# Optimization experiments

Measured on AMD Instinct MI355X. Metric: run time of the kernel, lower is better.

Reference implementation:

```python
import jax, jax.numpy as jnp
import numpy as np

N, E, G = 30000, 60000, 1200
EMB, HID, OUT = 768, 384, 768
NEG = 0.01  # leaky_relu negative slope (torch default / GATConv negative_slope)


def _seg_softmax(a, idx, num):
    m = jax.ops.segment_max(a, idx, num_segments=num)
    e = jnp.exp(a - m[idx])
    s = jax.ops.segment_sum(e, idx, num_segments=num)
    return e / (s[idx] + 1e-16)


def _gru(x, h, Wi, Wh, bi, bh):
    gi = x @ Wi + bi
    gh = h @ Wh + bh
    ir, iz, in_ = jnp.split(gi, 3, -1)
    hr, hz, hn = jnp.split(gh, 3, -1)
    r = jax.nn.sigmoid(ir + hr)
    z = jax.nn.sigmoid(iz + hz)
    n = jnp.tanh(in_ + r * hn)
    return (1.0 - z) * n + z * h


def setup_inputs() -> dict:
    key = jax.random.key(0)
    ks = iter(jax.random.split(key, 64))
    def W(*shape):
        return jax.random.normal(next(ks), shape, jnp.float32) / np.sqrt(shape[0])
    z = lambda *s: jnp.zeros(s, jnp.float32)
    inp = {}
    inp['x_idx'] = jax.random.randint(next(ks), (N, 9), 0, 178)
    inp['edge_index'] = jax.random.randint(next(ks), (2, E), 0, N)
    inp['edge_attr_idx'] = jax.random.randint(next(ks), (E, 3), 0, 18)
    inp['batch'] = jnp.sort(jax.random.randint(next(ks), (N,), 0, G))
    inp['x_emb'] = W(178, EMB)
    inp['e_emb'] = W(18, EMB)
    inp['lin1_W'] = W(EMB, HID); inp['lin1_b'] = z(HID)
    inp['att_l'] = W(HID); inp['att_r'] = W(HID)
    inp['gl1_W'] = W(HID + EMB, HID); inp['gl2_W'] = W(HID, HID); inp['gate_b'] = z(HID)
    inp['gru1_Wi'] = W(HID, 3 * HID); inp['gru1_Wh'] = W(HID, 3 * HID)
    inp['gru1_bi'] = z(3 * HID); inp['gru1_bh'] = z(3 * HID)
    inp['gat_W'] = W(HID, HID); inp['gat_as'] = W(HID); inp['gat_ad'] = W(HID); inp['gat_b'] = z(HID)
    inp['gru2_Wi'] = W(HID, 3 * HID); inp['gru2_Wh'] = W(HID, 3 * HID)
    inp['gru2_bi'] = z(3 * HID); inp['gru2_bh'] = z(3 * HID)
    inp['mol_W'] = W(HID, HID); inp['mol_as'] = W(HID); inp['mol_ad'] = W(HID); inp['mol_b'] = z(HID)
    inp['mgru_Wi'] = W(HID, 3 * HID); inp['mgru_Wh'] = W(HID, 3 * HID)
    inp['mgru_bi'] = z(3 * HID); inp['mgru_bh'] = z(3 * HID)
    inp['lin2_W'] = W(HID, OUT); inp['lin2_b'] = z(OUT)
    return inp


def reference(x_idx, edge_index, edge_attr_idx, batch,
              x_emb, e_emb, lin1_W, lin1_b,
              att_l, att_r, gl1_W, gl2_W, gate_b,
              gru1_Wi, gru1_Wh, gru1_bi, gru1_bh,
              gat_W, gat_as, gat_ad, gat_b,
              gru2_Wi, gru2_Wh, gru2_bi, gru2_bh,
              mol_W, mol_as, mol_ad, mol_b,
              mgru_Wi, mgru_Wh, mgru_bi, mgru_bh,
              lin2_W, lin2_b):
    src, dst = edge_index[0], edge_index[1]
    # embedding-sum over feature columns
    x = x_emb[x_idx].sum(1)            # [N, EMB]
    ea = e_emb[edge_attr_idx].sum(1)   # [E, EMB]
    x = jax.nn.leaky_relu(x @ lin1_W + lin1_b, NEG)  # [N, HID]
    # --- GATEConv (edge-attr attention) ---
    m = jax.nn.leaky_relu(jnp.concatenate([x[src], ea], -1) @ gl1_W, NEG)  # [E, HID]
    a = jax.nn.leaky_relu(m @ att_l + x[dst] @ att_r, NEG)
    a = _seg_softmax(a, dst, N)
    h = jax.ops.segment_sum((m @ gl2_W) * a[:, None], dst, num_segments=N) + gate_b
    x = jax.nn.relu(_gru(jax.nn.elu(h), x, gru1_Wi, gru1_Wh, gru1_bi, gru1_bh))
    # --- atom GATConv (num_layers=2 -> one extra layer, heads=1, no self-loops) ---
    xl = x @ gat_W
    a = jax.nn.leaky_relu((xl @ gat_as)[src] + (xl @ gat_ad)[dst], NEG)
    a = _seg_softmax(a, dst, N)
    h = jax.ops.segment_sum(xl[src] * a[:, None], dst, num_segments=N) + gat_b
    x = jax.nn.relu(_gru(jax.nn.elu(h), x, gru2_Wi, gru2_Wh, gru2_bi, gru2_bh))
    # --- attentive molecule readout, num_timesteps=3 ---
    out = jax.nn.relu(jax.ops.segment_sum(x, batch, num_segments=G))  # [G, HID]
    xl = x @ mol_W
    a_node = xl @ mol_as  # per-node source attention term (fixed across timesteps)
    for _ in range(3):
        a_g = (out @ mol_W) @ mol_ad
        a = jax.nn.leaky_relu(a_node + a_g[batch], NEG)
        a = _seg_softmax(a, batch, G)
        h = jax.ops.segment_sum(xl * a[:, None], batch, num_segments=G) + mol_b
        out = jax.nn.relu(_gru(jax.nn.elu(h), out, mgru_Wi, mgru_Wh, mgru_bi, mgru_bh))
    return out @ lin2_W + lin2_b  # [G, OUT]
```

## Files before the change

### kernel.cpp

```cpp
#include <hip/hip_runtime.h>
#include <cstdint>
#include <cstddef>

#define NN 30000
#define NE 60000
#define NG 1200
#define HID 384
#define EMB 768
#define OUTD 768
#define NEGS 0.01f

typedef _Float16 f16;
typedef _Float16 f16x8 __attribute__((ext_vector_type(8)));
typedef float f32x16 __attribute__((ext_vector_type(16)));

static __device__ __forceinline__ float leaky(float x){ return x > 0.f ? x : NEGS * x; }
static __device__ __forceinline__ float elu1(float x){ return x > 0.f ? x : (expf(x) - 1.f); }
static __device__ __forceinline__ float sigm(float x){ return 1.f / (1.f + expf(-x)); }

static __device__ __forceinline__ size_t pf_idx(int row, int col){
  return (((((size_t)(row >> 5)) * 24 + (col >> 4)) * 2 + ((col >> 3) & 1)) * 32
          + (row & 31)) * 8 + (col & 7);
}
#define PF_RB_STRIDE 12288
#define PF_KS_STRIDE 512
#define PF_GATE_STRIDE 147456

__global__ __launch_bounds__(256) void k_gemm(
    const float* __restrict__ A, const float* __restrict__ B,
    const float* __restrict__ bias, float* __restrict__ C,
    int M, int N, int K, int act)
{
  __shared__ float As[16][65];
  __shared__ float Bs[16][65];
  const int tid = threadIdx.x;
  const int tx = tid & 15, ty = tid >> 4;
  const int row0 = blockIdx.y * 64, col0 = blockIdx.x * 64;
  const int ar = tid >> 2, ak = (tid & 3) << 2;
  const int bk = tid >> 4, bc = (tid & 15) << 2;
  float acc[4][4] = {};
  for (int k0 = 0; k0 < K; k0 += 16) {
    float4 av = make_float4(0.f, 0.f, 0.f, 0.f);
    if (row0 + ar < M)
      av = *(const float4*)(A + (size_t)(row0 + ar) * K + k0 + ak);
    As[ak + 0][ar] = av.x; As[ak + 1][ar] = av.y;
    As[ak + 2][ar] = av.z; As[ak + 3][ar] = av.w;
    float4 bv = *(const float4*)(B + (size_t)(k0 + bk) * N + col0 + bc);
    Bs[bk][bc + 0] = bv.x; Bs[bk][bc + 1] = bv.y;
    Bs[bk][bc + 2] = bv.z; Bs[bk][bc + 3] = bv.w;
    __syncthreads();
#pragma unroll
    for (int kk = 0; kk < 16; kk++) {
      float a[4], b[4];
#pragma unroll
      for (int i = 0; i < 4; i++) a[i] = As[kk][(ty << 2) + i];
#pragma unroll
      for (int j = 0; j < 4; j++) b[j] = Bs[kk][(tx << 2) + j];
#pragma unroll
      for (int i = 0; i < 4; i++)
#pragma unroll
        for (int j = 0; j < 4; j++)
          acc[i][j] = fmaf(a[i], b[j], acc[i][j]);
    }
    __syncthreads();
  }
#pragma unroll
  for (int i = 0; i < 4; i++) {
    int r = row0 + (ty << 2) + i;
    if (r >= M) continue;
#pragma unroll
    for (int j = 0; j < 4; j++) {
      int c = col0 + (tx << 2) + j;
      float v = acc[i][j];
      if (bias) v += bias[c];
      if (act == 1) v = leaky(v);
      else if (act == 2) v = elu1(v);
      else if (act == 3) v = fmaxf(v, 0.f);
      C[(size_t)r * N + c] = v;
    }
  }
}

__global__ __launch_bounds__(256) void k_hgemm(
    const f16* __restrict__ Apf, const f16* __restrict__ Bpf,
    const float* __restrict__ bias, float* __restrict__ Cf, f16* __restrict__ Ch,
    int M, int Nn, int act)
{
  const int nct = Nn >> 7;
  const int id = blockIdx.x;
  const int lane8 = id & 7, chunk = id >> 3;
  const int ct = chunk % nct, rg = chunk / nct;
  const int rt = rg * 8 + lane8;
  const int Mt = (M + 127) >> 7;
  if (rt >= Mt) return;
  const int r0 = rt * 128, n0 = ct * 128;
  const int tid = threadIdx.x;
  const int wid = tid >> 6, lane = tid & 63;
  const int wr = wid >> 1, wc = wid & 1;
  const int l31 = lane & 31, lhi = lane >> 5;
  const size_t lane_off = (size_t)(lhi * 32 + l31) * 8;
  const f16* pA[2]; const f16* pB[2];
#pragma unroll
  for (int i = 0; i < 2; i++) {
    pA[i] = Apf + (size_t)(r0 / 32 + wr * 2 + i) * PF_RB_STRIDE + lane_off;
    pB[i] = Bpf + (size_t)(n0 / 32 + wc * 2 + i) * PF_RB_STRIDE + lane_off;
  }
  f32x16 acc[2][2];
#pragma unroll
  for (int i = 0; i < 2; i++)
#pragma unroll
    for (int j = 0; j < 2; j++)
#pragma unroll
      for (int r = 0; r < 16; r++) acc[i][j][r] = 0.f;
  f16x8 af[2], bf[2], naf[2], nbf[2];
#pragma unroll
  for (int i = 0; i < 2; i++) { af[i] = *(const f16x8*)(pA[i]); bf[i] = *(const f16x8*)(pB[i]); }
#pragma unroll 4
  for (int ks = 0; ks < 24; ks++) {
    const size_t noff = (size_t)(ks < 23 ? ks + 1 : 23) * PF_KS_STRIDE;
#pragma unroll
    for (int i = 0; i < 2; i++) { naf[i] = *(const f16x8*)(pA[i] + noff); nbf[i] = *(const f16x8*)(pB[i] + noff); }
#pragma unroll
    for (int i = 0; i < 2; i++)
#pragma unroll
      for (int j = 0; j < 2; j++)
        acc[i][j] = __builtin_amdgcn_mfma_f32_32x32x16_f16(af[i], bf[j], acc[i][j], 0, 0, 0);
#pragma unroll
    for (int i = 0; i < 2; i++) { af[i] = naf[i]; bf[i] = nbf[i]; }
  }
#pragma unroll
  for (int i = 0; i < 2; i++)
#pragma unroll
    for (int j = 0; j < 2; j++) {
      int col = n0 + wc * 64 + j * 32 + l31;
      float bv = bias ? bias[col] : 0.f;
#pragma unroll
      for (int r = 0; r < 16; r++) {
        int row = r0 + wr * 64 + i * 32 + (r & 3) + 8 * (r >> 2) + 4 * lhi;
        if (row < M) {
          float v = acc[i][j][r] + bv;
          if (act == 1) v = leaky(v);
          else if (act == 2) v = elu1(v);
          else if (act == 3) v = fmaxf(v, 0.f);
          if (Cf) Cf[(size_t)row * Nn + col] = v;
          if (Ch) Ch[pf_idx(row, col)] = (f16)v;
        }
      }
    }
}

__global__ __launch_bounds__(256) void k_gru_hgemm(
    const f16* __restrict__ Upf, const f16* __restrict__ Hpf,
    const f16* __restrict__ Wip, const f16* __restrict__ Whp,
    const float* __restrict__ bi, const float* __restrict__ bh,
    float* __restrict__ Xo, f16* __restrict__ Xoh, int M)
{
  const int id = blockIdx.x;
  const int lane8 = id & 7, chunk = id >> 3;
  const int ct = chunk % 6, rg = chunk / 6;
  const int rt = rg * 8 + lane8;
  const int Mt = (M + 63) >> 6;
  if (rt >= Mt) return;
  const int r0 = rt * 64, c0 = ct * 64;
  const int tid = threadIdx.x;
  const int wid = tid >> 6, lane = tid & 63;
  const int wr = wid >> 1, wc = wid & 1;
  const int l31 = lane & 31, lhi = lane >> 5;
  const size_t lane_off = (size_t)(lhi * 32 + l31) * 8;
  const f16* pU  = Upf + (size_t)(r0 / 32 + wr) * PF_RB_STRIDE + lane_off;
  const f16* pH  = Hpf + (size_t)(r0 / 32 + wr) * PF_RB_STRIDE + lane_off;
  const f16* pWi = Wip + (size_t)(c0 / 32 + wc) * PF_RB_STRIDE + lane_off;
  const f16* pWh = Whp + (size_t)(c0 / 32 + wc) * PF_RB_STRIDE + lane_off;
#define Z16 {0,0,0,0,0,0,0,0,0,0,0,0,0,0,0,0}
  f32x16 accR = Z16, accZ = Z16, aN = Z16, hN = Z16;
  f16x8 au, ah, bir, biz, bin, bhr, bhz, bhn;
  f16x8 nau, nah, nbir, nbiz, nbin, nbhr, nbhz, nbhn;
  au  = *(const f16x8*)(pU);
  ah  = *(const f16x8*)(pH);
  bir = *(const f16x8*)(pWi);
  biz = *(const f16x8*)(pWi + PF_GATE_STRIDE);
  bin = *(const f16x8*)(pWi + 2 * PF_GATE_STRIDE);
  bhr = *(const f16x8*)(pWh);
  bhz = *(const f16x8*)(pWh + PF_GATE_STRIDE);
  bhn = *(const f16x8*)(pWh + 2 * PF_GATE_STRIDE);
#pragma unroll 4
  for (int ks = 0; ks < 24; ks++) {
    const size_t noff = (size_t)(ks < 23 ? ks + 1 : 23) * PF_KS_STRIDE;
    nau  = *(const f16x8*)(pU + noff);
    nah  = *(const f16x8*)(pH + noff);
    nbir = *(const f16x8*)(pWi + noff);
    nbiz = *(const f16x8*)(pWi + PF_GATE_STRIDE + noff);
    nbin = *(const f16x8*)(pWi + 2 * PF_GATE_STRIDE + noff);
    nbhr = *(const f16x8*)(pWh + noff);
    nbhz = *(const f16x8*)(pWh + PF_GATE_STRIDE + noff);
    nbhn = *(const f16x8*)(pWh + 2 * PF_GATE_STRIDE + noff);
    accR = __builtin_amdgcn_mfma_f32_32x32x16_f16(au, bir, accR, 0, 0, 0);
    accR = __builtin_amdgcn_mfma_f32_32x32x16_f16(ah, bhr, accR, 0, 0, 0);
    accZ = __builtin_amdgcn_mfma_f32_32x32x16_f16(au, biz, accZ, 0, 0, 0);
    accZ = __builtin_amdgcn_mfma_f32_32x32x16_f16(ah, bhz, accZ, 0, 0, 0);
    aN   = __builtin_amdgcn_mfma_f32_32x32x16_f16(au, bin, aN, 0, 0, 0);
    hN   = __builtin_amdgcn_mfma_f32_32x32x16_f16(ah, bhn, hN, 0, 0, 0);
    au = nau; ah = nah; bir = nbir; biz = nbiz; bin = nbin;
    bhr = nbhr; bhz = nbhz; bhn = nbhn;
  }
  const int col = c0 + wc * 32 + l31;
  const float brz = bi[col] + bh[col];
  const float bzz = bi[HID + col] + bh[HID + col];
  const float bin_ = bi[2 * HID + col];
  const float bhn_ = bh[2 * HID + col];
#pragma unroll
  for (int r = 0; r < 16; r++) {
    int row = r0 + wr * 32 + (r & 3) + 8 * (r >> 2) + 4 * lhi;
    if (row < M) {
      float rg_ = sigm(accR[r] + brz);
      float zg  = sigm(accZ[r] + bzz);
      float ng  = tanhf(aN[r] + bin_ + rg_ * (hN[r] + bhn_));
      float hp  = (float)Hpf[pf_idx(row, col)];
      float o = (1.f - zg) * ng + zg * hp;
      o = fmaxf(o, 0.f);
      if (Xo) Xo[(size_t)row * HID + col] = o;
      Xoh[pf_idx(row, col)] = (f16)o;
    }
  }
}

__global__ void k_wpack_all(
    const float* __restrict__ w0, const float* __restrict__ w1,
    const float* __restrict__ w2, const float* __restrict__ w3,
    const float* __restrict__ w4, const float* __restrict__ w5,
    const float* __restrict__ w6, const float* __restrict__ w7,
    const float* __restrict__ w8, const float* __restrict__ w9,
    const float* __restrict__ w10,
    f16* __restrict__ d0, f16* __restrict__ d1, f16* __restrict__ d2,
    f16* __restrict__ d3, f16* __restrict__ d4, f16* __restrict__ d5,
    f16* __restrict__ d6, f16* __restrict__ d7, f16* __restrict__ d8,
    f16* __restrict__ d9, f16* __restrict__ d10)
{
  long t = (long)blockIdx.x * blockDim.x + threadIdx.x;
  if (t >= 3538944L) return;
  const float* W; f16* Wp; int Nn; long tt;
  if (t < 589824L) {
    int s = (int)(t / 147456L); tt = t - (long)s * 147456L; Nn = HID;
    if (s == 0) { W = w0; Wp = d0; } else if (s == 1) { W = w1; Wp = d1; }
    else if (s == 2) { W = w2; Wp = d2; } else { W = w3; Wp = d3; }
  } else if (t < 3244032L) {
    long u = t - 589824L;
    int s = (int)(u / 442368L); tt = u - (long)s * 442368L; Nn = 3 * HID;
    if (s == 0) { W = w4; Wp = d4; } else if (s == 1) { W = w5; Wp = d5; }
    else if (s == 2) { W = w6; Wp = d6; } else if (s == 3) { W = w7; Wp = d7; }
    else if (s == 4) { W = w8; Wp = d8; } else { W = w9; Wp = d9; }
  } else {
    tt = t - 3244032L; Nn = OUTD; W = w10; Wp = d10;
  }
  int elem = (int)(tt & 7); long c = tt >> 3;
  int l31 = (int)(c & 31); long q = c >> 5;
  int lhi = (int)(q & 1); long p = q >> 1;
  int ks = (int)(p % 24); int rb = (int)(p / 24);
  int n = rb * 32 + l31, k = ks * 16 + lhi * 8 + elem;
  Wp[tt] = (f16)W[(size_t)k * Nn + n];
}

__global__ void k_node_embed2(const int* __restrict__ xi, const float* __restrict__ T1,
                              const float* __restrict__ b, const float* __restrict__ att_r,
                              f16* __restrict__ x1h, float* __restrict__ xr, int n)
{
  int w = (int)(((long)blockIdx.x * blockDim.x + threadIdx.x) >> 6);
  int lane = threadIdx.x & 63;
  if (w >= n) return;
  int idx[9];
#pragma unroll
  for (int j = 0; j < 9; j++) idx[j] = xi[w * 9 + j];
  float s = 0.f;
#pragma unroll
  for (int t = 0; t < 6; t++) {
    int c = lane + 64 * t;
    float v = b[c];
#pragma unroll
    for (int j = 0; j < 9; j++) v += T1[(size_t)idx[j] * HID + c];
    v = leaky(v);
    x1h[pf_idx(w, c)] = (f16)v;
    s += v * att_r[c];
  }
  for (int o = 32; o; o >>= 1) s += __shfl_down(s, o, 64);
  if (lane == 0) xr[w] = s;
}

__global__ void k_rowdot(const float* __restrict__ X, const float* __restrict__ v,
                         float* __restrict__ out, int M)
{
  int w = (int)(((long)blockIdx.x * blockDim.x + threadIdx.x) >> 6);
  int lane = threadIdx.x & 63;
  if (w >= M) return;
  float s = 0.f;
  for (int j = lane; j < HID; j += 64) s += X[(size_t)w * HID + j] * v[j];
  for (int o = 32; o; o >>= 1) s += __shfl_down(s, o, 64);
  if (lane == 0) out[w] = s;
}

__global__ void k_rowdot2(const float* __restrict__ X, const float* __restrict__ v1,
                          const float* __restrict__ v2, float* __restrict__ o1,
                          float* __restrict__ o2, int M)
{
  int w = (int)(((long)blockIdx.x * blockDim.x + threadIdx.x) >> 6);
  int lane = threadIdx.x & 63;
  if (w >= M) return;
  float s1 = 0.f, s2 = 0.f;
  for (int j = lane; j < HID; j += 64) {
    float x = X[(size_t)w * HID + j];
    s1 += x * v1[j]; s2 += x * v2[j];
  }
  for (int o = 32; o; o >>= 1) { s1 += __shfl_down(s1, o, 64); s2 += __shfl_down(s2, o, 64); }
  if (lane == 0) { o1[w] = s1; o2[w] = s2; }
}

__global__ void k_gbounds(const int* __restrict__ batch, int* __restrict__ gstart, int n, int G)
{
  int g = (int)((long)blockIdx.x * blockDim.x + threadIdx.x);
  if (g > G) return;
  int lo = 0, hi = n;
  while (lo < hi) { int mid = (lo + hi) >> 1; if (batch[mid] < g) lo = mid + 1; else hi = mid; }
  gstart[g] = lo;
}

__global__ void k_deg(const int* __restrict__ dst, int* __restrict__ cnt, int ne)
{
  int e = (int)((long)blockIdx.x * blockDim.x + threadIdx.x);
  if (e >= ne) return;
  atomicAdd(&cnt[dst[e]], 1);
}

__global__ __launch_bounds__(1024) void k_scan(const int* __restrict__ cnt,
                                               int* __restrict__ rowptr,
                                               int* __restrict__ cursor)
{
  __shared__ int part[1024];
  const int tid = threadIdx.x;
  const int c0 = tid * 30, c1 = min(c0 + 30, NN);
  int s = 0;
  for (int i = c0; i < c1; i++) s += cnt[i];
  part[tid] = s;
  __syncthreads();
  for (int o = 1; o < 1024; o <<= 1) {
    int v = (tid >= o) ? part[tid - o] : 0;
    __syncthreads();
    part[tid] += v;
    __syncthreads();
  }
  int run = (tid ? part[tid - 1] : 0);
  for (int i = c0; i < c1; i++) { rowptr[i] = run; cursor[i] = run; run += cnt[i]; }
  if (tid == 1023) rowptr[NN] = part[1023];
}

__global__ void k_fill(const int* __restrict__ dst, int* __restrict__ cursor,
                       int* __restrict__ elist, int ne)
{
  int e = (int)((long)blockIdx.x * blockDim.x + threadIdx.x);
  if (e >= ne) return;
  int p = atomicAdd(&cursor[dst[e]], 1);
  elist[p] = e;
}

__global__ void k_gate_agg(const float* __restrict__ P, const float* __restrict__ Te,
                           const int* __restrict__ ei, const int* __restrict__ eai,
                           const float* __restrict__ attl, const float* __restrict__ xr,
                           const int* __restrict__ rowptr, const int* __restrict__ elist,
                           f16* __restrict__ Hout, int n)
{
  int node = (int)(((long)blockIdx.x * blockDim.x + threadIdx.x) >> 6);
  int lane = threadIdx.x & 63;
  if (node >= n) return;
  const int e0 = rowptr[node], e1 = rowptr[node + 1];
  const float xrd = xr[node];
  float h0 = 0.f, h1 = 0.f, h2 = 0.f, h3 = 0.f, h4 = 0.f, h5 = 0.f;
  float mx = -3.4e38f, s = 0.f;
  for (int q = e0; q < e1; q++) {
    int e = elist[q];
    int src = ei[e];
    int i0 = eai[e * 3], i1 = eai[e * 3 + 1], i2 = eai[e * 3 + 2];
    float m[6];
    float dot = 0.f;
#pragma unroll
    for (int t = 0; t < 6; t++) {
      int c = lane + 64 * t;
      float v = P[(size_t)src * HID + c] + Te[(size_t)i0 * HID + c]
              + Te[(size_t)i1 * HID + c] + Te[(size_t)i2 * HID + c];
      v = leaky(v);
      m[t] = v;
      dot += v * attl[c];
    }
#pragma unroll
    for (int o = 32; o; o >>= 1) dot += __shfl_xor(dot, o, 64);
    float a = leaky(dot + xrd);
    if (a > mx) {
      float f = expf(mx - a);
      s *= f; h0 *= f; h1 *= f; h2 *= f; h3 *= f; h4 *= f; h5 *= f;
      mx = a;
    }
    float w = expf(a - mx);
    s += w;
    h0 += w * m[0]; h1 += w * m[1]; h2 += w * m[2];
    h3 += w * m[3]; h4 += w * m[4]; h5 += w * m[5];
  }
  const float inv = 1.f / (s + 1e-16f);
  Hout[pf_idx(node, lane)]           = (f16)(h0 * inv);
  Hout[pf_idx(node, lane + 64)]      = (f16)(h1 * inv);
  Hout[pf_idx(node, lane + 128)]     = (f16)(h2 * inv);
  Hout[pf_idx(node, lane + 192)]     = (f16)(h3 * inv);
  Hout[pf_idx(node, lane + 256)]     = (f16)(h4 * inv);
  Hout[pf_idx(node, lane + 320)]     = (f16)(h5 * inv);
}

__global__ void k_gat_agg(const float* __restrict__ XL, const int* __restrict__ ei,
                          const float* __restrict__ sS, const float* __restrict__ sD,
                          const float* __restrict__ gat_b,
                          const int* __restrict__ rowptr, const int* __restrict__ elist,
                          f16* __restrict__ Hout, int n)
{
  int node = (int)(((long)blockIdx.x * blockDim.x + threadIdx.x) >> 6);
  int lane = threadIdx.x & 63;
  if (node >= n) return;
  const int e0 = rowptr[node], e1 = rowptr[node + 1];
  const float sDn = sD[node];
  float h0 = 0.f, h1 = 0.f, h2 = 0.f, h3 = 0.f, h4 = 0.f, h5 = 0.f;
  float mx = -3.4e38f, s = 0.f;
  for (int q = e0; q < e1; q++) {
    int e = elist[q];
    int src = ei[e];
    float a = leaky(sS[src] + sDn);
    if (a > mx) {
      float f = expf(mx - a);
      s *= f; h0 *= f; h1 *= f; h2 *= f; h3 *= f; h4 *= f; h5 *= f;
      mx = a;
    }
    float w = expf(a - mx);
    s += w;
    const float* row = XL + (size_t)src * HID;
    h0 += w * row[lane];
    h1 += w * row[lane + 64];
    h2 += w * row[lane + 128];
    h3 += w * row[lane + 192];
    h4 += w * row[lane + 256];
    h5 += w * row[lane + 320];
  }
  const float inv = 1.f / (s + 1e-16f);
  Hout[pf_idx(node, lane)]       = (f16)elu1(h0 * inv + gat_b[lane]);
  Hout[pf_idx(node, lane + 64)]  = (f16)elu1(h1 * inv + gat_b[lane + 64]);
  Hout[pf_idx(node, lane + 128)] = (f16)elu1(h2 * inv + gat_b[lane + 128]);
  Hout[pf_idx(node, lane + 192)] = (f16)elu1(h3 * inv + gat_b[lane + 192]);
  Hout[pf_idx(node, lane + 256)] = (f16)elu1(h4 * inv + gat_b[lane + 256]);
  Hout[pf_idx(node, lane + 320)] = (f16)elu1(h5 * inv + gat_b[lane + 320]);
}

__global__ __launch_bounds__(384) void k_graph_sum(const float* __restrict__ X,
                                                   const int* __restrict__ gstart,
                                                   float* __restrict__ OUTa,
                                                   f16* __restrict__ OUTaPF)
{
  const int g = blockIdx.x;
  const int tid = threadIdx.x;
  const int s0 = gstart[g], s1 = gstart[g + 1];
  float acc = 0.f;
  for (int i = s0; i < s1; i++) acc += X[(size_t)i * HID + tid];
  acc = fmaxf(acc, 0.f);
  OUTa[(size_t)g * HID + tid] = acc;
  OUTaPF[pf_idx(g, tid)] = (f16)acc;
}

__global__ __launch_bounds__(384) void k_mol_iter(
    const float* __restrict__ cur, const float* __restrict__ XLm,
    const float* __restrict__ a_node, const float* __restrict__ w_g,
    const float* __restrict__ mol_b, const int* __restrict__ gstart,
    f16* __restrict__ HMp)
{
  const int g = blockIdx.x;
  const int tid = threadIdx.x;
  const int lane = tid & 63, wv = tid >> 6;
  __shared__ float red[6];
  __shared__ float wbuf[384];
  __shared__ float sh[3];
  const int s0 = gstart[g], s1 = gstart[g + 1];
  float p = cur[(size_t)g * HID + tid] * w_g[tid];
  for (int o = 32; o; o >>= 1) p += __shfl_down(p, o, 64);
  if (lane == 0) red[wv] = p;
  __syncthreads();
  if (tid == 0) { float s = 0.f; for (int i = 0; i < 6; i++) s += red[i]; sh[0] = s; }
  __syncthreads();
  const float ag = sh[0];
  float mx = -3.4e38f;
  for (int n = s0 + tid; n < s1; n += 384) mx = fmaxf(mx, leaky(a_node[n] + ag));
  for (int o = 32; o; o >>= 1) mx = fmaxf(mx, __shfl_down(mx, o, 64));
  __syncthreads();
  if (lane == 0) red[wv] = mx;
  __syncthreads();
  if (tid == 0) { float m = red[0]; for (int i = 1; i < 6; i++) m = fmaxf(m, red[i]); sh[1] = m; }
  __syncthreads();
  const float gmx = sh[1];
  float sm = 0.f;
  for (int n = s0 + tid; n < s1; n += 384) sm += expf(leaky(a_node[n] + ag) - gmx);
  for (int o = 32; o; o >>= 1) sm += __shfl_down(sm, o, 64);
  __syncthreads();
  if (lane == 0) red[wv] = sm;
  __syncthreads();
  if (tid == 0) { float s = 0.f; for (int i = 0; i < 6; i++) s += red[i]; sh[2] = s; }
  __syncthreads();
  const float inv = 1.f / (sh[2] + 1e-16f);
  float h = 0.f;
  for (int base = s0; base < s1; base += 384) {
    int cnt = min(384, s1 - base);
    __syncthreads();
    if (tid < cnt) wbuf[tid] = expf(leaky(a_node[base + tid] + ag) - gmx) * inv;
    __syncthreads();
    for (int k = 0; k < cnt; k++) h += XLm[(size_t)(base + k) * HID + tid] * wbuf[k];
  }
  h = elu1(h + mol_b[tid]);
  HMp[pf_idx(g, tid)] = (f16)h;
}

extern "C" void kernel_launch(void* const* d_in, const int* in_sizes, int n_in,
                              void* d_out, int out_size, void* d_ws, size_t ws_size,
                              hipStream_t stream)
{
  const int* x_idx = (const int*)d_in[0];
  const int* edge_index = (const int*)d_in[1];
  const int* eai = (const int*)d_in[2];
  const int* batch = (const int*)d_in[3];
  const float* x_emb = (const float*)d_in[4];
  const float* e_emb = (const float*)d_in[5];
  const float* lin1_W = (const float*)d_in[6];
  const float* lin1_b = (const float*)d_in[7];
  const float* att_l = (const float*)d_in[8];
  const float* att_r = (const float*)d_in[9];
  const float* gl1_W = (const float*)d_in[10];
  const float* gl2_W = (const float*)d_in[11];
  const float* gate_b = (const float*)d_in[12];
  const float* gru1_Wi = (const float*)d_in[13];
  const float* gru1_Wh = (const float*)d_in[14];
  const float* gru1_bi = (const float*)d_in[15];
  const float* gru1_bh = (const float*)d_in[16];
  const float* gat_W = (const float*)d_in[17];
  const float* gat_as = (const float*)d_in[18];
  const float* gat_ad = (const float*)d_in[19];
  const float* gat_b = (const float*)d_in[20];
  const float* gru2_Wi = (const float*)d_in[21];
  const float* gru2_Wh = (const float*)d_in[22];
  const float* gru2_bi = (const float*)d_in[23];
  const float* gru2_bh = (const float*)d_in[24];
  const float* mol_W = (const float*)d_in[25];
  const float* mol_as = (const float*)d_in[26];
  const float* mol_ad = (const float*)d_in[27];
  const float* mol_b = (const float*)d_in[28];
  const float* mgru_Wi = (const float*)d_in[29];
  const float* mgru_Wh = (const float*)d_in[30];
  const float* mgru_bi = (const float*)d_in[31];
  const float* mgru_bh = (const float*)d_in[32];
  const float* lin2_W = (const float*)d_in[33];
  const float* lin2_b = (const float*)d_in[34];
  float* outp = (float*)d_out;

  const size_t NB = (size_t)NN * HID;
  const size_t GB = (size_t)NG * HID;
  const size_t PFH = (size_t)940 * PF_RB_STRIDE;
  const size_t PFG = (size_t)40 * PF_RB_STRIDE;

  float* ws = (float*)d_ws;
  size_t off = 0;
  auto alloc = [&](size_t n) { float* p = ws + off; off += n; return p; };
  auto alloch = [&](size_t n) { f16* p = (f16*)(ws + off); off += (n + 1) / 2; return p; };
  float* A    = alloc(NB);
  float* B    = alloc(NB);
  f16* H1 = alloch(PFH);
  f16* H2 = alloch(PFH);
  f16* H3 = alloch(PFH);
  f16* W1p   = alloch((size_t)HID * HID);
  f16* W2p   = alloch((size_t)HID * HID);
  f16* Wgatp = alloch((size_t)HID * HID);
  f16* Wmolp = alloch((size_t)HID * HID);
  f16* Wg1ip = alloch((size_t)3 * HID * HID);
  f16* Wg1hp = alloch((size_t)3 * HID * HID);
  f16* Wg2ip = alloch((size_t)3 * HID * HID);
  f16* Wg2hp = alloch((size_t)3 * HID * HID);
  f16* Wmgip = alloch((size_t)3 * HID * HID);
  f16* Wmghp = alloch((size_t)3 * HID * HID);
  f16* Wl2p  = alloch((size_t)HID * OUTD);
  f16* OUTaPF = alloch(PFG);
  f16* OUTbPF = alloch(PFG);
  f16* HMp    = alloch(PFG);
  float* T1   = alloc((size_t)178 * HID);
  float* Te   = alloc((size_t)18 * HID);
  float* w_g  = alloc(HID);
  float* xr   = alloc(NN);
  float* sS   = alloc(NN);
  float* sD   = alloc(NN);
  float* a_node = alloc(NN);
  float* OUTa = alloc(GB);
  float* OUTb = alloc(GB);
  int* gstart = (int*)alloc(NG + 2);
  int* cnt    = (int*)alloc(NN);
  int* rowptr = (int*)alloc(NN + 2);
  int* cursor = (int*)alloc(NN);
  int* elist  = (int*)alloc(NE);
  (void)n_in; (void)in_sizes; (void)out_size;
  if (ws_size < off * sizeof(float)) return;

  const int* dstArr = edge_index + NE;
  dim3 blk(256);
  auto g1 = [](long n) { return dim3((unsigned)((n + 255) / 256)); };
  auto gw = [](long waves) { return dim3((unsigned)((waves * 64 + 255) / 256)); };
  const int MtH = (NN + 127) / 128;
  const dim3 gH((unsigned)(8 * 3 * ((MtH + 7) / 8)));
  const int MtR = (NN + 63) / 64;
  const dim3 gR((unsigned)(8 * 6 * ((MtR + 7) / 8)));
  const int MtGH = (NG + 127) / 128;
  const dim3 gF((unsigned)(8 * 6 * ((MtGH + 7) / 8)));
  const int MtGR = (NG + 63) / 64;
  const dim3 gRG((unsigned)(8 * 6 * ((MtGR + 7) / 8)));

  hipLaunchKernelGGL(k_wpack_all, g1(3538944L), blk, 0, stream,
                     gl1_W, gl2_W, gat_W, mol_W,
                     gru1_Wi, gru1_Wh, gru2_Wi, gru2_Wh, mgru_Wi, mgru_Wh, lin2_W,
                     W1p, W2p, Wgatp, Wmolp,
                     Wg1ip, Wg1hp, Wg2ip, Wg2hp, Wmgip, Wmghp, Wl2p);
  hipLaunchKernelGGL(k_gemm, dim3(HID / 64, 3), blk, 0, stream,
                     x_emb, lin1_W, nullptr, T1, 178, HID, EMB, 0);
  hipLaunchKernelGGL(k_gemm, dim3(HID / 64, 1), blk, 0, stream,
                     e_emb, gl1_W + (size_t)HID * HID, nullptr, Te, 18, HID, EMB, 0);
  hipLaunchKernelGGL(k_rowdot, gw(HID), blk, 0, stream, mol_W, mol_ad, w_g, HID);
  hipLaunchKernelGGL(k_gbounds, g1(NG + 1), blk, 0, stream, batch, gstart, NN, NG);
  hipMemsetAsync(cnt, 0, NN * sizeof(int), stream);
  hipLaunchKernelGGL(k_deg, g1(NE), blk, 0, stream, dstArr, cnt, NE);
  hipLaunchKernelGGL(k_scan, dim3(1), dim3(1024), 0, stream, cnt, rowptr, cursor);
  hipLaunchKernelGGL(k_fill, g1(NE), blk, 0, stream, dstArr, cursor, elist, NE);

  hipLaunchKernelGGL(k_node_embed2, gw(NN), blk, 0, stream, x_idx, T1, lin1_b, att_r, H1, xr, NN);

  hipLaunchKernelGGL(k_hgemm, gH, blk, 0, stream, H1, W1p, nullptr, B, (f16*)nullptr, NN, HID, 0);
  hipLaunchKernelGGL(k_gate_agg, gw(NN), blk, 0, stream, B, Te, edge_index, eai, att_l, xr,
                     rowptr, elist, H2, NN);
  hipLaunchKernelGGL(k_hgemm, gH, blk, 0, stream, H2, W2p, gate_b, (float*)nullptr, H3, NN, HID, 2);
  hipLaunchKernelGGL(k_gru_hgemm, gR, blk, 0, stream, H3, H1, Wg1ip, Wg1hp,
                     gru1_bi, gru1_bh, (float*)nullptr, H2, NN);

  hipLaunchKernelGGL(k_hgemm, gH, blk, 0, stream, H2, Wgatp, nullptr, B, (f16*)nullptr, NN, HID, 0);
  hipLaunchKernelGGL(k_rowdot2, gw(NN), blk, 0, stream, B, gat_as, gat_ad, sS, sD, NN);
  hipLaunchKernelGGL(k_gat_agg, gw(NN), blk, 0, stream, B, edge_index, sS, sD, gat_b,
                     rowptr, elist, H1, NN);
  hipLaunchKernelGGL(k_gru_hgemm, gR, blk, 0, stream, H1, H2, Wg2ip, Wg2hp,
                     gru2_bi, gru2_bh, B, H3, NN);

  hipLaunchKernelGGL(k_graph_sum, dim3(NG), dim3(384), 0, stream, B, gstart, OUTa, OUTaPF);
  hipLaunchKernelGGL(k_hgemm, gH, blk, 0, stream, H3, Wmolp, nullptr, A, (f16*)nullptr, NN, HID, 0);
  hipLaunchKernelGGL(k_rowdot, gw(NN), blk, 0, stream, A, mol_as, a_node, NN);

  float* cur = OUTa;   f16* curPF = OUTaPF;
  float* nxt = OUTb;   f16* nxtPF = OUTbPF;
  for (int t = 0; t < 3; t++) {
    hipLaunchKernelGGL(k_mol_iter, dim3(NG), dim3(384), 0, stream,
                       cur, A, a_node, w_g, mol_b, gstart, HMp);
    hipLaunchKernelGGL(k_gru_hgemm, gRG, blk, 0, stream, HMp, curPF, Wmgip, Wmghp,
                       mgru_bi, mgru_bh, nxt, nxtPF, NG);
    float* tf = cur; cur = nxt; nxt = tf;
    f16* th = curPF; curPF = nxtPF; nxtPF = th;
  }

  hipLaunchKernelGGL(k_hgemm, gF, blk, 0, stream, curPF, Wl2p, lin2_b, outp, (f16*)nullptr, NG, OUTD, 0);
}
```

Baseline: 795.2 us.

## Fuse attention row-dot products into GEMM epilogue and deepen GRU A-prefetch

```diff
diff --git a/kernel.cpp b/kernel.cpp
--- a/kernel.cpp
+++ b/kernel.cpp
@@ -84,7 +84,9 @@
 __global__ __launch_bounds__(256) void k_hgemm(
     const f16* __restrict__ Apf, const f16* __restrict__ Bpf,
     const float* __restrict__ bias, float* __restrict__ Cf, f16* __restrict__ Ch,
-    int M, int Nn, int act)
+    int M, int Nn, int act,
+    const float* __restrict__ dv1, const float* __restrict__ dv2,
+    float* __restrict__ od1, float* __restrict__ od2)
 {
   const int nct = Nn >> 7;
   const int id = blockIdx.x;
@@ -147,6 +149,29 @@
         }
       }
     }
+  if (od1) {
+    const float w1a = dv1[n0 + wc * 64 + l31];
+    const float w1b = dv1[n0 + wc * 64 + 32 + l31];
+    const float w2a = dv2 ? dv2[n0 + wc * 64 + l31] : 0.f;
+    const float w2b = dv2 ? dv2[n0 + wc * 64 + 32 + l31] : 0.f;
+#pragma unroll
+    for (int i = 0; i < 2; i++)
+#pragma unroll
+      for (int r = 0; r < 16; r++) {
+        int row = r0 + wr * 64 + i * 32 + (r & 3) + 8 * (r >> 2) + 4 * lhi;
+        float p1 = acc[i][0][r] * w1a + acc[i][1][r] * w1b;
+        float p2 = acc[i][0][r] * w2a + acc[i][1][r] * w2b;
+#pragma unroll
+        for (int o = 16; o; o >>= 1) {
+          p1 += __shfl_xor(p1, o, 64);
+          p2 += __shfl_xor(p2, o, 64);
+        }
+        if (l31 == 0 && row < M) {
+          atomicAdd(&od1[row], p1);
+          if (od2) atomicAdd(&od2[row], p2);
+        }
+      }
+  }
 }
 
 __global__ __launch_bounds__(256) void k_gru_hgemm(
@@ -173,10 +198,11 @@
   const f16* pWh = Whp + (size_t)(c0 / 32 + wc) * PF_RB_STRIDE + lane_off;
 #define Z16 {0,0,0,0,0,0,0,0,0,0,0,0,0,0,0,0}
   f32x16 accR = Z16, accZ = Z16, aN = Z16, hN = Z16;
-  f16x8 au, ah, bir, biz, bin, bhr, bhz, bhn;
-  f16x8 nau, nah, nbir, nbiz, nbin, nbhr, nbhz, nbhn;
-  au  = *(const f16x8*)(pU);
-  ah  = *(const f16x8*)(pH);
+  f16x8 au0, ah0, au1, ah1, bir, biz, bin, bhr, bhz, bhn;
+  au0 = *(const f16x8*)(pU);
+  ah0 = *(const f16x8*)(pH);
+  au1 = *(const f16x8*)(pU + PF_KS_STRIDE);
+  ah1 = *(const f16x8*)(pH + PF_KS_STRIDE);
   bir = *(const f16x8*)(pWi);
   biz = *(const f16x8*)(pWi + PF_GATE_STRIDE);
   bin = *(const f16x8*)(pWi + 2 * PF_GATE_STRIDE);
@@ -185,22 +211,24 @@
   bhn = *(const f16x8*)(pWh + 2 * PF_GATE_STRIDE);
 #pragma unroll 4
   for (int ks = 0; ks < 24; ks++) {
-    const size_t noff = (size_t)(ks < 23 ? ks + 1 : 23) * PF_KS_STRIDE;
-    nau  = *(const f16x8*)(pU + noff);
-    nah  = *(const f16x8*)(pH + noff);
-    nbir = *(const f16x8*)(pWi + noff);
-    nbiz = *(const f16x8*)(pWi + PF_GATE_STRIDE + noff);
-    nbin = *(const f16x8*)(pWi + 2 * PF_GATE_STRIDE + noff);
-    nbhr = *(const f16x8*)(pWh + noff);
-    nbhz = *(const f16x8*)(pWh + PF_GATE_STRIDE + noff);
-    nbhn = *(const f16x8*)(pWh + 2 * PF_GATE_STRIDE + noff);
-    accR = __builtin_amdgcn_mfma_f32_32x32x16_f16(au, bir, accR, 0, 0, 0);
-    accR = __builtin_amdgcn_mfma_f32_32x32x16_f16(ah, bhr, accR, 0, 0, 0);
-    accZ = __builtin_amdgcn_mfma_f32_32x32x16_f16(au, biz, accZ, 0, 0, 0);
-    accZ = __builtin_amdgcn_mfma_f32_32x32x16_f16(ah, bhz, accZ, 0, 0, 0);
-    aN   = __builtin_amdgcn_mfma_f32_32x32x16_f16(au, bin, aN, 0, 0, 0);
-    hN   = __builtin_amdgcn_mfma_f32_32x32x16_f16(ah, bhn, hN, 0, 0, 0);
-    au = nau; ah = nah; bir = nbir; biz = nbiz; bin = nbin;
+    const size_t woff = (size_t)(ks < 23 ? ks + 1 : 23) * PF_KS_STRIDE;
+    const size_t aoff = (size_t)(ks < 22 ? ks + 2 : 23) * PF_KS_STRIDE;
+    f16x8 nau  = *(const f16x8*)(pU + aoff);
+    f16x8 nah  = *(const f16x8*)(pH + aoff);
+    f16x8 nbir = *(const f16x8*)(pWi + woff);
+    f16x8 nbiz = *(const f16x8*)(pWi + PF_GATE_STRIDE + woff);
+    f16x8 nbin = *(const f16x8*)(pWi + 2 * PF_GATE_STRIDE + woff);
+    f16x8 nbhr = *(const f16x8*)(pWh + woff);
+    f16x8 nbhz = *(const f16x8*)(pWh + PF_GATE_STRIDE + woff);
+    f16x8 nbhn = *(const f16x8*)(pWh + 2 * PF_GATE_STRIDE + woff);
+    accR = __builtin_amdgcn_mfma_f32_32x32x16_f16(au0, bir, accR, 0, 0, 0);
+    accR = __builtin_amdgcn_mfma_f32_32x32x16_f16(ah0, bhr, accR, 0, 0, 0);
+    accZ = __builtin_amdgcn_mfma_f32_32x32x16_f16(au0, biz, accZ, 0, 0, 0);
+    accZ = __builtin_amdgcn_mfma_f32_32x32x16_f16(ah0, bhz, accZ, 0, 0, 0);
+    aN   = __builtin_amdgcn_mfma_f32_32x32x16_f16(au0, bin, aN, 0, 0, 0);
+    hN   = __builtin_amdgcn_mfma_f32_32x32x16_f16(ah0, bhn, hN, 0, 0, 0);
+    au0 = au1; ah0 = ah1; au1 = nau; ah1 = nah;
+    bir = nbir; biz = nbiz; bin = nbin;
     bhr = nbhr; bhz = nbhz; bhn = nbhn;
   }
   const int col = c0 + wc * 32 + l31;
@@ -295,22 +323,6 @@
   for (int j = lane; j < HID; j += 64) s += X[(size_t)w * HID + j] * v[j];
   for (int o = 32; o; o >>= 1) s += __shfl_down(s, o, 64);
   if (lane == 0) out[w] = s;
-}
-
-__global__ void k_rowdot2(const float* __restrict__ X, const float* __restrict__ v1,
-                          const float* __restrict__ v2, float* __restrict__ o1,
-                          float* __restrict__ o2, int M)
-{
-  int w = (int)(((long)blockIdx.x * blockDim.x + threadIdx.x) >> 6);
-  int lane = threadIdx.x & 63;
-  if (w >= M) return;
-  float s1 = 0.f, s2 = 0.f;
-  for (int j = lane; j < HID; j += 64) {
-    float x = X[(size_t)w * HID + j];
-    s1 += x * v1[j]; s2 += x * v2[j];
-  }
-  for (int o = 32; o; o >>= 1) { s1 += __shfl_down(s1, o, 64); s2 += __shfl_down(s2, o, 64); }
-  if (lane == 0) { o1[w] = s1; o2[w] = s2; }
 }
 
 __global__ void k_gbounds(const int* __restrict__ batch, int* __restrict__ gstart, int n, int G)
@@ -614,6 +626,8 @@
   const dim3 gF((unsigned)(8 * 6 * ((MtGH + 7) / 8)));
   const int MtGR = (NG + 63) / 64;
   const dim3 gRG((unsigned)(8 * 6 * ((MtGR + 7) / 8)));
+  const float* FN = nullptr;
+  float* FNm = nullptr;
 
   hipLaunchKernelGGL(k_wpack_all, g1(3538944L), blk, 0, stream,
                      gl1_W, gl2_W, gat_W, mol_W,
@@ -630,26 +644,29 @@
   hipLaunchKernelGGL(k_deg, g1(NE), blk, 0, stream, dstArr, cnt, NE);
   hipLaunchKernelGGL(k_scan, dim3(1), dim3(1024), 0, stream, cnt, rowptr, cursor);
   hipLaunchKernelGGL(k_fill, g1(NE), blk, 0, stream, dstArr, cursor, elist, NE);
+  hipMemsetAsync(sS, 0, 3 * NN * sizeof(float), stream);
 
   hipLaunchKernelGGL(k_node_embed2, gw(NN), blk, 0, stream, x_idx, T1, lin1_b, att_r, H1, xr, NN);
 
-  hipLaunchKernelGGL(k_hgemm, gH, blk, 0, stream, H1, W1p, nullptr, B, (f16*)nullptr, NN, HID, 0);
+  hipLaunchKernelGGL(k_hgemm, gH, blk, 0, stream, H1, W1p, FN, B, (f16*)nullptr, NN, HID, 0,
+                     FN, FN, FNm, FNm);
   hipLaunchKernelGGL(k_gate_agg, gw(NN), blk, 0, stream, B, Te, edge_index, eai, att_l, xr,
                      rowptr, elist, H2, NN);
-  hipLaunchKernelGGL(k_hgemm, gH, blk, 0, stream, H2, W2p, gate_b, (float*)nullptr, H3, NN, HID, 2);
+  hipLaunchKernelGGL(k_hgemm, gH, blk, 0, stream, H2, W2p, gate_b, (float*)nullptr, H3, NN, HID, 2,
+                     FN, FN, FNm, FNm);
   hipLaunchKernelGGL(k_gru_hgemm, gR, blk, 0, stream, H3, H1, Wg1ip, Wg1hp,
                      gru1_bi, gru1_bh, (float*)nullptr, H2, NN);
 
-  hipLaunchKernelGGL(k_hgemm, gH, blk, 0, stream, H2, Wgatp, nullptr, B, (f16*)nullptr, NN, HID, 0);
-  hipLaunchKernelGGL(k_rowdot2, gw(NN), blk, 0, stream, B, gat_as, gat_ad, sS, sD, NN);
+  hipLaunchKernelGGL(k_hgemm, gH, blk, 0, stream, H2, Wgatp, FN, B, (f16*)nullptr, NN, HID, 0,
+                     gat_as, gat_ad, sS, sD);
   hipLaunchKernelGGL(k_gat_agg, gw(NN), blk, 0, stream, B, edge_index, sS, sD, gat_b,
                      rowptr, elist, H1, NN);
   hipLaunchKernelGGL(k_gru_hgemm, gR, blk, 0, stream, H1, H2, Wg2ip, Wg2hp,
                      gru2_bi, gru2_bh, B, H3, NN);
 
   hipLaunchKernelGGL(k_graph_sum, dim3(NG), dim3(384), 0, stream, B, gstart, OUTa, OUTaPF);
-  hipLaunchKernelGGL(k_hgemm, gH, blk, 0, stream, H3, Wmolp, nullptr, A, (f16*)nullptr, NN, HID, 0);
-  hipLaunchKernelGGL(k_rowdot, gw(NN), blk, 0, stream, A, mol_as, a_node, NN);
+  hipLaunchKernelGGL(k_hgemm, gH, blk, 0, stream, H3, Wmolp, FN, A, (f16*)nullptr, NN, HID, 0,
+                     mol_as, FN, a_node, FNm);
 
   float* cur = OUTa;   f16* curPF = OUTaPF;
   float* nxt = OUTb;   f16* nxtPF = OUTbPF;
@@ -662,5 +679,6 @@
     f16* th = curPF; curPF = nxtPF; nxtPF = th;
   }
 
-  hipLaunchKernelGGL(k_hgemm, gF, blk, 0, stream, curPF, Wl2p, lin2_b, outp, (f16*)nullptr, NG, OUTD, 0);
-}
+  hipLaunchKernelGGL(k_hgemm, gF, blk, 0, stream, curPF, Wl2p, lin2_b, outp, (f16*)nullptr,
+                     NG, OUTD, 0, FN, FN, FNm, FNm);
+}
```

Measured after the change: 846.2 us. 6.4% more time.
